# Performance work log

Measured on AMD Instinct MI355X. Metric: run time of the kernel, lower is better.

## Reference

```python
import jax, jax.numpy as jnp
import numpy as np

B, T, D = 2, 2048, 1024
H, DH = 16, 64  # d_model = n_heads * d_head


def setup_inputs() -> dict:
    key = jax.random.key(0)
    k1, k2, k3 = jax.random.split(key, 3)
    x = jax.random.normal(k1, (B, T, D), dtype=jnp.float32)
    # torch Linear(d_model, 3*H*DH, bias=False): store transposed so y = x @ W
    Wqkv = jax.random.normal(k2, (D, 3 * H * DH), dtype=jnp.float32) * (D ** -0.5)
    Wo = jax.random.normal(k3, (H * DH, D), dtype=jnp.float32) * ((H * DH) ** -0.5)
    mask = jnp.ones((B, T), dtype=jnp.float32)  # key padding mask
    return {"x": x, "Wqkv": Wqkv, "Wo": Wo, "mask": mask}


def reference(x, Wqkv, Wo, mask):
    b, t, _ = x.shape
    scale = DH ** -0.5
    qkv = (x @ Wqkv).reshape(b, t, 3, H, DH)
    q = jnp.moveaxis(qkv[:, :, 0], 1, 2)  # [B,H,T,DH]
    k = jnp.moveaxis(qkv[:, :, 1], 1, 2)
    v = jnp.moveaxis(qkv[:, :, 2], 1, 2)
    scores = jnp.einsum('bhqd,bhkd->bhqk', q, k) * scale  # [B,H,T,T]
    causal = jnp.tril(jnp.ones((t, t), dtype=x.dtype))
    # faithful to source: multiply by mask, then fill masked positions with -inf
    scores = scores * causal
    scores = jnp.where(causal == 0, -jnp.inf, scores)
    am = mask[:, None, None, :]  # [B,1,1,T]
    scores = scores * am
    scores = jnp.where(am == 0, -jnp.inf, scores)
    p = jax.nn.softmax(scores, axis=-1)
    p = jnp.where(jnp.isnan(p), jnp.zeros_like(p), p)  # NaN cleanup
    out = jnp.einsum('bhqk,bhkd->bhqd', p, v)
    out = jnp.moveaxis(out, 1, 2).reshape(b, t, H * DH)
    return out @ Wo
```

## Files before the change

### kernel.cpp

```cpp
#include <hip/hip_runtime.h>
#include <math.h>

#define B_ 2
#define T_ 2048
#define D_ 1024
#define H_ 16
#define DH_ 64
#define NROWS (B_ * T_)
#define QKV_N (3 * H_ * DH_)

typedef __attribute__((ext_vector_type(8))) short short8v;
typedef __attribute__((ext_vector_type(4))) float f32x4;

#define SWZ(row) ((((row) & 7) ^ (((row) >> 3) & 7)))
#define GSWZ(row) (((row) >> 1) & 3)

static __device__ __forceinline__ unsigned short f2bf(float x) {
    unsigned u = __float_as_uint(x);
    u = (u + 0x7FFFu + ((u >> 16) & 1u)) >> 16;
    return (unsigned short)u;
}
static __device__ __forceinline__ int packbf(float lo, float hi) {
    return (int)((unsigned)f2bf(lo) | ((unsigned)f2bf(hi) << 16));
}

__global__ __launch_bounds__(256)
void f32_to_bf16_k(const float* __restrict__ in, unsigned short* __restrict__ out,
                   int n8)
{
    const int i = blockIdx.x * 256 + threadIdx.x;
    if (i >= n8) return;
    const float4* p = (const float4*)in;
    float4 a = p[2 * i], b = p[2 * i + 1];
    int4 w;
    w.x = packbf(a.x, a.y); w.y = packbf(a.z, a.w);
    w.z = packbf(b.x, b.y); w.w = packbf(b.z, b.w);
    ((int4*)out)[i] = w;
}

__global__ __launch_bounds__(256)
void transpose_bf16_k(const float* __restrict__ in, unsigned short* __restrict__ out,
                      int R, int C)
{
    __shared__ float tile[64][65];
    const int r0 = blockIdx.y * 64, c0 = blockIdx.x * 64;
    const int tr = threadIdx.x >> 4;
    const int tc = (threadIdx.x & 15) * 4;
#pragma unroll
    for (int rr = 0; rr < 64; rr += 16) {
        float4 v = *(const float4*)(in + (size_t)(r0 + tr + rr) * C + c0 + tc);
        tile[tr + rr][tc + 0] = v.x; tile[tr + rr][tc + 1] = v.y;
        tile[tr + rr][tc + 2] = v.z; tile[tr + rr][tc + 3] = v.w;
    }
    __syncthreads();
    const int ow = threadIdx.x >> 2;
    const int os = (threadIdx.x & 3) * 16;
    int4 w0, w1;
    float s[16];
#pragma unroll
    for (int e = 0; e < 16; ++e) s[e] = tile[os + e][ow];
    w0.x = packbf(s[0], s[1]);   w0.y = packbf(s[2], s[3]);
    w0.z = packbf(s[4], s[5]);   w0.w = packbf(s[6], s[7]);
    w1.x = packbf(s[8], s[9]);   w1.y = packbf(s[10], s[11]);
    w1.z = packbf(s[12], s[13]); w1.w = packbf(s[14], s[15]);
    unsigned short* orow = out + (size_t)(c0 + ow) * R + r0 + os;
    *(int4*)(orow) = w0;
    *(int4*)(orow + 8) = w1;
}

__global__ __launch_bounds__(256)
void gemm_bt_bf16(const unsigned short* __restrict__ A,
                  const unsigned short* __restrict__ Bt,
                  float* __restrict__ C, int M, int N, int K)
{
    __shared__ __align__(16) unsigned short As[2][128 * 32];
    __shared__ __align__(16) unsigned short Bs[2][128 * 32];

    const int tid = threadIdx.x;
    const int w = tid >> 6, l = tid & 63;
    const int lhi = l >> 4, llo = l & 15;
    const int wr = w >> 1, wc = w & 1;
    const int bm = blockIdx.y * 128, bn = blockIdx.x * 128;

    const int srow = w * 32 + (l >> 2);
    const int sg   = l & 3;

    const unsigned short* Ab = A + (size_t)bm * K;
    const unsigned short* Bb = Bt + (size_t)bn * K;

    f32x4 acc[4][4];
#pragma unroll
    for (int mi = 0; mi < 4; ++mi)
#pragma unroll
        for (int ni = 0; ni < 4; ++ni) acc[mi][ni] = (f32x4){0.f, 0.f, 0.f, 0.f};

    short8v a0r, a1r, b0r, b1r;
    const int nt = K >> 5;

#define LOADT(t) do {                                                        \
        const size_t ko = (size_t)(t) * 32 + sg * 8;                         \
        a0r = *(const short8v*)(Ab + (size_t)srow * K + ko);                 \
        a1r = *(const short8v*)(Ab + (size_t)(srow + 16) * K + ko);         \
        b0r = *(const short8v*)(Bb + (size_t)srow * K + ko);                 \
        b1r = *(const short8v*)(Bb + (size_t)(srow + 16) * K + ko);         \
    } while (0)
#define WRITET(buf) do {                                                     \
        *(short8v*)&As[buf][srow * 32 + (sg ^ GSWZ(srow)) * 8] = a0r;        \
        *(short8v*)&As[buf][(srow + 16) * 32 + (sg ^ GSWZ(srow + 16)) * 8] = a1r; \
        *(short8v*)&Bs[buf][srow * 32 + (sg ^ GSWZ(srow)) * 8] = b0r;        \
        *(short8v*)&Bs[buf][(srow + 16) * 32 + (sg ^ GSWZ(srow + 16)) * 8] = b1r; \
    } while (0)

    LOADT(0);
    WRITET(0);
    __syncthreads();

    int cur = 0;
    for (int t = 0; t < nt; ++t) {
        if (t + 1 < nt) LOADT(t + 1);

        short8v af[4], bf[4];
#pragma unroll
        for (int mi = 0; mi < 4; ++mi) {
            const int m = wr * 64 + mi * 16 + llo;
            af[mi] = *(const short8v*)&As[cur][m * 32 + (lhi ^ GSWZ(m)) * 8];
        }
#pragma unroll
        for (int ni = 0; ni < 4; ++ni) {
            const int n = wc * 64 + ni * 16 + llo;
            bf[ni] = *(const short8v*)&Bs[cur][n * 32 + (lhi ^ GSWZ(n)) * 8];
        }
#pragma unroll
        for (int mi = 0; mi < 4; ++mi)
#pragma unroll
            for (int ni = 0; ni < 4; ++ni)
                acc[mi][ni] = __builtin_amdgcn_mfma_f32_16x16x32_bf16(
                    af[mi], bf[ni], acc[mi][ni], 0, 0, 0);

        if (t + 1 < nt) WRITET(cur ^ 1);
        __syncthreads();
        cur ^= 1;
    }
#undef LOADT
#undef WRITET

#pragma unroll
    for (int mi = 0; mi < 4; ++mi)
#pragma unroll
        for (int ni = 0; ni < 4; ++ni) {
            const int col = bn + wc * 64 + ni * 16 + llo;
            const int rb = bm + wr * 64 + mi * 16 + lhi * 4;
#pragma unroll
            for (int i = 0; i < 4; ++i)
                C[(size_t)(rb + i) * N + col] = acc[mi][ni][i];
        }
}

__global__ __launch_bounds__(256)
void attn_mfma(const float* __restrict__ qkv, const float* __restrict__ mask,
               unsigned short* __restrict__ out)
{
    __shared__ __align__(16) unsigned short Ks[64 * 64];
    __shared__ __align__(16) unsigned short Vt[64 * 64];
    __shared__ __align__(16) unsigned short Pl[4][16 * 64];
    __shared__ float ms[64];

    const int tid = threadIdx.x;
    const int w   = tid >> 6;
    const int l   = tid & 63;
    const int lhi = l >> 4;
    const int llo = l & 15;
    const int b = blockIdx.z;
    const int h = blockIdx.y;

    const int sr  = tid >> 2;
    const int sg0 = (tid & 3) * 2;

    for (int qsel = 0; qsel < 2; ++qsel) {
        const int qt = qsel ? (31 - (int)blockIdx.x) : (int)blockIdx.x;
        const int qb = qt * 64;

        short8v qf[2];
        {
            const float* qrow = qkv + (size_t)(b * T_ + qb + w * 16 + llo) * QKV_N
                                + h * DH_;
#pragma unroll
            for (int kc = 0; kc < 2; ++kc) {
                const float* src = qrow + kc * 32 + lhi * 8;
                float4 c0 = *(const float4*)(src);
                float4 c1 = *(const float4*)(src + 4);
                float v[8] = {c0.x, c0.y, c0.z, c0.w, c1.x, c1.y, c1.z, c1.w};
#pragma unroll
                for (int e = 0; e < 8; ++e)
                    qf[kc][e] = (short)f2bf(v[e] * 0.125f);
            }
        }

        f32x4 acc[4];
#pragma unroll
        for (int ct = 0; ct < 4; ++ct) acc[ct] = (f32x4){0.f, 0.f, 0.f, 0.f};
        float mrow[4] = {-INFINITY, -INFINITY, -INFINITY, -INFINITY};
        float lrow[4] = {0.f, 0.f, 0.f, 0.f};

        for (int t0 = 0; t0 <= qt; ++t0) {
            const int k0 = t0 * 64;
            {
                const float* kbase = qkv + (size_t)(b * T_ + k0 + sr) * QKV_N
                                     + H_ * DH_ + h * DH_;
#pragma unroll
                for (int s = 0; s < 2; ++s) {
                    const int g = sg0 + s;
                    float4 ka = *(const float4*)(kbase + g * 8);
                    float4 kb = *(const float4*)(kbase + g * 8 + 4);
                    int4 wk;
                    wk.x = packbf(ka.x, ka.y); wk.y = packbf(ka.z, ka.w);
                    wk.z = packbf(kb.x, kb.y); wk.w = packbf(kb.z, kb.w);
                    *(int4*)&Ks[(sr * 8 + (g ^ SWZ(sr))) * 8] = wk;

                    float4 va = *(const float4*)(kbase + H_ * DH_ + g * 8);
                    float4 vb = *(const float4*)(kbase + H_ * DH_ + g * 8 + 4);
                    float vv[8] = {va.x, va.y, va.z, va.w, vb.x, vb.y, vb.z, vb.w};
#pragma unroll
                    for (int e = 0; e < 8; ++e) {
                        const int dr = g * 8 + e;
                        Vt[(dr * 8 + ((sr >> 3) ^ SWZ(dr))) * 8 + (sr & 7)] =
                            f2bf(vv[e]);
                    }
                }
                if (tid < 64) ms[tid] = mask[b * T_ + k0 + tid];
            }
            __syncthreads();

            float p[4][4];
#pragma unroll
            for (int ct = 0; ct < 4; ++ct) {
                f32x4 a = (f32x4){0.f, 0.f, 0.f, 0.f};
#pragma unroll
                for (int kc = 0; kc < 2; ++kc) {
                    const int row = ct * 16 + llo;
                    const int G = kc * 4 + lhi;
                    short8v kf = *(const short8v*)&Ks[(row * 8 + (G ^ SWZ(row))) * 8];
                    a = __builtin_amdgcn_mfma_f32_16x16x32_bf16(qf[kc], kf, a, 0, 0, 0);
                }
                const int kg = k0 + ct * 16 + llo;
                const float amv = ms[ct * 16 + llo];
#pragma unroll
                for (int i = 0; i < 4; ++i) {
                    const int qg = qb + w * 16 + lhi * 4 + i;
                    const float s = a[i] * amv;
                    p[ct][i] = (kg <= qg && amv != 0.f) ? s : -INFINITY;
                }
            }

            float corr[4], meff[4];
#pragma unroll
            for (int i = 0; i < 4; ++i) {
                float mx = fmaxf(fmaxf(p[0][i], p[1][i]), fmaxf(p[2][i], p[3][i]));
                mx = fmaxf(mx, __shfl_xor(mx, 1));
                mx = fmaxf(mx, __shfl_xor(mx, 2));
                mx = fmaxf(mx, __shfl_xor(mx, 4));
                mx = fmaxf(mx, __shfl_xor(mx, 8));
                const float mn = fmaxf(mrow[i], mx);
                meff[i] = (mn > -INFINITY) ? mn : 0.f;
                corr[i] = __expf(mrow[i] - meff[i]);
                mrow[i] = mn;
            }
#pragma unroll
            for (int i = 0; i < 4; ++i) {
#pragma unroll
                for (int ct = 0; ct < 4; ++ct)
                    p[ct][i] = __expf(p[ct][i] - meff[i]);
                float sm = (p[0][i] + p[1][i]) + (p[2][i] + p[3][i]);
                sm += __shfl_xor(sm, 1);
                sm += __shfl_xor(sm, 2);
                sm += __shfl_xor(sm, 4);
                sm += __shfl_xor(sm, 8);
                lrow[i] = corr[i] * lrow[i] + sm;
#pragma unroll
                for (int ct2 = 0; ct2 < 4; ++ct2)
                    acc[ct2][i] *= corr[i];
            }

            unsigned short* pw = Pl[w];
#pragma unroll
            for (int ct = 0; ct < 4; ++ct) {
                const int c = ct * 16 + llo;
#pragma unroll
                for (int i = 0; i < 4; ++i) {
                    const int r = lhi * 4 + i;
                    pw[(r * 8 + ((c >> 3) ^ SWZ(r))) * 8 + (c & 7)] = f2bf(p[ct][i]);
                }
            }
            asm volatile("s_waitcnt lgkmcnt(0)" ::: "memory");
            __builtin_amdgcn_sched_barrier(0);
            short8v pf[2];
#pragma unroll
            for (int kc = 0; kc < 2; ++kc) {
                const int G = kc * 4 + lhi;
                pf[kc] = *(const short8v*)&pw[(llo * 8 + (G ^ SWZ(llo))) * 8];
            }

#pragma unroll
            for (int ct2 = 0; ct2 < 4; ++ct2) {
#pragma unroll
                for (int kc = 0; kc < 2; ++kc) {
                    const int row = ct2 * 16 + llo;
                    const int G = kc * 4 + lhi;
                    short8v vf = *(const short8v*)&Vt[(row * 8 + (G ^ SWZ(row))) * 8];
                    acc[ct2] = __builtin_amdgcn_mfma_f32_16x16x32_bf16(
                        pf[kc], vf, acc[ct2], 0, 0, 0);
                }
            }
            __syncthreads();
        }

#pragma unroll
        for (int i = 0; i < 4; ++i) {
            const float invl = (lrow[i] > 0.f) ? 1.f / lrow[i] : 0.f;
            const int qg = qb + w * 16 + lhi * 4 + i;
            unsigned short* orow = out + (size_t)(b * T_ + qg) * (H_ * DH_) + h * DH_;
#pragma unroll
            for (int ct2 = 0; ct2 < 4; ++ct2)
                orow[ct2 * 16 + llo] = f2bf(acc[ct2][i] * invl);
        }
    }
}

extern "C" void kernel_launch(void* const* d_in, const int* in_sizes, int n_in,
                              void* d_out, int out_size, void* d_ws, size_t ws_size,
                              hipStream_t stream)
{
    const float* x    = (const float*)d_in[0];
    const float* Wqkv = (const float*)d_in[1];
    const float* Wo   = (const float*)d_in[2];
    const float* mask = (const float*)d_in[3];
    float* out = (float*)d_out;

    char* p = (char*)d_ws;
    float* qkv = (float*)p;                 p += (size_t)NROWS * QKV_N * 4;
    unsigned short* xb      = (unsigned short*)p; p += (size_t)NROWS * D_ * 2;
    unsigned short* wqkv_t  = (unsigned short*)p; p += (size_t)QKV_N * D_ * 2;
    unsigned short* wo_t    = (unsigned short*)p; p += (size_t)D_ * D_ * 2;
    unsigned short* attnb   = (unsigned short*)p;

    f32_to_bf16_k<<<(NROWS * D_ / 8 + 255) / 256, 256, 0, stream>>>(
        x, xb, NROWS * D_ / 8);
    transpose_bf16_k<<<dim3(QKV_N / 64, D_ / 64), 256, 0, stream>>>(
        Wqkv, wqkv_t, D_, QKV_N);
    transpose_bf16_k<<<dim3(D_ / 64, D_ / 64), 256, 0, stream>>>(
        Wo, wo_t, D_, D_);

    gemm_bt_bf16<<<dim3(QKV_N / 128, NROWS / 128), 256, 0, stream>>>(
        xb, wqkv_t, qkv, NROWS, QKV_N, D_);

    attn_mfma<<<dim3(16, H_, B_), 256, 0, stream>>>(qkv, mask, attnb);

    gemm_bt_bf16<<<dim3(D_ / 128, NROWS / 128), 256, 0, stream>>>(
        attnb, wo_t, out, NROWS, D_, H_ * DH_);
}
```

Measured before the change: 251.4 us.

## Fuse QKV epilogue into bf16 head-major Q/K/Vt layouts and prefetch K/V in attention

The QKV GEMM now writes bf16 Q (pre-scaled), K, and transposed V in per-head contiguous layouts instead of a fp32 interleaved buffer. The attention kernel reads these directly with vector loads, register-prefetches the next K/V tile while computing, and launches one q-tile per block (32 blocks in x) instead of pairing two q-tiles per block. This cuts fp32 traffic and per-tile conversion/transposed scatter stores, at the cost of less coalesced epilogue stores in the GEMM and possible causal load imbalance across blocks.

```diff
diff --git a/kernel.cpp b/kernel.cpp
--- a/kernel.cpp
+++ b/kernel.cpp
@@ -69,9 +69,12 @@
 }
 
 __global__ __launch_bounds__(256)
-void gemm_bt_bf16(const unsigned short* __restrict__ A,
-                  const unsigned short* __restrict__ Bt,
-                  float* __restrict__ C, int M, int N, int K)
+void gemm_qkv(const unsigned short* __restrict__ A,
+              const unsigned short* __restrict__ Bt,
+              unsigned short* __restrict__ Qb,
+              unsigned short* __restrict__ Kb,
+              unsigned short* __restrict__ Vtb,
+              int M, int N, int K)
 {
     __shared__ __align__(16) unsigned short As[2][128 * 32];
     __shared__ __align__(16) unsigned short Bs[2][128 * 32];
@@ -118,8 +121,7 @@
     int cur = 0;
     for (int t = 0; t < nt; ++t) {
         if (t + 1 < nt) LOADT(t + 1);
-
-        short8v af[4], bf[4];
+        short8v af[4], bfr[4];
 #pragma unroll
         for (int mi = 0; mi < 4; ++mi) {
             const int m = wr * 64 + mi * 16 + llo;
@@ -128,15 +130,14 @@
 #pragma unroll
         for (int ni = 0; ni < 4; ++ni) {
             const int n = wc * 64 + ni * 16 + llo;
-            bf[ni] = *(const short8v*)&Bs[cur][n * 32 + (lhi ^ GSWZ(n)) * 8];
+            bfr[ni] = *(const short8v*)&Bs[cur][n * 32 + (lhi ^ GSWZ(n)) * 8];
         }
 #pragma unroll
         for (int mi = 0; mi < 4; ++mi)
 #pragma unroll
             for (int ni = 0; ni < 4; ++ni)
                 acc[mi][ni] = __builtin_amdgcn_mfma_f32_16x16x32_bf16(
-                    af[mi], bf[ni], acc[mi][ni], 0, 0, 0);
-
+                    af[mi], bfr[ni], acc[mi][ni], 0, 0, 0);
         if (t + 1 < nt) WRITET(cur ^ 1);
         __syncthreads();
         cur ^= 1;
@@ -149,6 +150,107 @@
 #pragma unroll
         for (int ni = 0; ni < 4; ++ni) {
             const int col = bn + wc * 64 + ni * 16 + llo;
+            const int rb  = bm + wr * 64 + mi * 16 + lhi * 4;
+            const int hh = (col >> 6) & 15;
+            const int dh = col & 63;
+            const int bb = rb >> 11;
+            const int tt = rb & 2047;
+            const int which = col >> 10;
+            if (which == 2) {
+                int2 pk;
+                pk.x = packbf(acc[mi][ni][0], acc[mi][ni][1]);
+                pk.y = packbf(acc[mi][ni][2], acc[mi][ni][3]);
+                *(int2*)&Vtb[((size_t)(bb * H_ + hh) * DH_ + dh) * T_ + tt] = pk;
+            } else {
+                unsigned short* dst = (which == 0 ? Qb : Kb)
+                    + ((size_t)(bb * H_ + hh) * T_ + tt) * DH_ + dh;
+                const float sc = (which == 0) ? 0.125f : 1.f;
+#pragma unroll
+                for (int i = 0; i < 4; ++i)
+                    dst[(size_t)i * DH_] = f2bf(acc[mi][ni][i] * sc);
+            }
+        }
+}
+
+__global__ __launch_bounds__(256)
+void gemm_bt_bf16(const unsigned short* __restrict__ A,
+                  const unsigned short* __restrict__ Bt,
+                  float* __restrict__ C, int M, int N, int K)
+{
+    __shared__ __align__(16) unsigned short As[2][128 * 32];
+    __shared__ __align__(16) unsigned short Bs[2][128 * 32];
+
+    const int tid = threadIdx.x;
+    const int w = tid >> 6, l = tid & 63;
+    const int lhi = l >> 4, llo = l & 15;
+    const int wr = w >> 1, wc = w & 1;
+    const int bm = blockIdx.y * 128, bn = blockIdx.x * 128;
+
+    const int srow = w * 32 + (l >> 2);
+    const int sg   = l & 3;
+
+    const unsigned short* Ab = A + (size_t)bm * K;
+    const unsigned short* Bb = Bt + (size_t)bn * K;
+
+    f32x4 acc[4][4];
+#pragma unroll
+    for (int mi = 0; mi < 4; ++mi)
+#pragma unroll
+        for (int ni = 0; ni < 4; ++ni) acc[mi][ni] = (f32x4){0.f, 0.f, 0.f, 0.f};
+
+    short8v a0r, a1r, b0r, b1r;
+    const int nt = K >> 5;
+
+#define LOADT(t) do {                                                        \
+        const size_t ko = (size_t)(t) * 32 + sg * 8;                         \
+        a0r = *(const short8v*)(Ab + (size_t)srow * K + ko);                 \
+        a1r = *(const short8v*)(Ab + (size_t)(srow + 16) * K + ko);         \
+        b0r = *(const short8v*)(Bb + (size_t)srow * K + ko);                 \
+        b1r = *(const short8v*)(Bb + (size_t)(srow + 16) * K + ko);         \
+    } while (0)
+#define WRITET(buf) do {                                                     \
+        *(short8v*)&As[buf][srow * 32 + (sg ^ GSWZ(srow)) * 8] = a0r;        \
+        *(short8v*)&As[buf][(srow + 16) * 32 + (sg ^ GSWZ(srow + 16)) * 8] = a1r; \
+        *(short8v*)&Bs[buf][srow * 32 + (sg ^ GSWZ(srow)) * 8] = b0r;        \
+        *(short8v*)&Bs[buf][(srow + 16) * 32 + (sg ^ GSWZ(srow + 16)) * 8] = b1r; \
+    } while (0)
+
+    LOADT(0);
+    WRITET(0);
+    __syncthreads();
+
+    int cur = 0;
+    for (int t = 0; t < nt; ++t) {
+        if (t + 1 < nt) LOADT(t + 1);
+        short8v af[4], bfr[4];
+#pragma unroll
+        for (int mi = 0; mi < 4; ++mi) {
+            const int m = wr * 64 + mi * 16 + llo;
+            af[mi] = *(const short8v*)&As[cur][m * 32 + (lhi ^ GSWZ(m)) * 8];
+        }
+#pragma unroll
+        for (int ni = 0; ni < 4; ++ni) {
+            const int n = wc * 64 + ni * 16 + llo;
+            bfr[ni] = *(const short8v*)&Bs[cur][n * 32 + (lhi ^ GSWZ(n)) * 8];
+        }
+#pragma unroll
+        for (int mi = 0; mi < 4; ++mi)
+#pragma unroll
+            for (int ni = 0; ni < 4; ++ni)
+                acc[mi][ni] = __builtin_amdgcn_mfma_f32_16x16x32_bf16(
+                    af[mi], bfr[ni], acc[mi][ni], 0, 0, 0);
+        if (t + 1 < nt) WRITET(cur ^ 1);
+        __syncthreads();
+        cur ^= 1;
+    }
+#undef LOADT
+#undef WRITET
+
+#pragma unroll
+    for (int mi = 0; mi < 4; ++mi)
+#pragma unroll
+        for (int ni = 0; ni < 4; ++ni) {
+            const int col = bn + wc * 64 + ni * 16 + llo;
             const int rb = bm + wr * 64 + mi * 16 + lhi * 4;
 #pragma unroll
             for (int i = 0; i < 4; ++i)
@@ -156,173 +258,166 @@
         }
 }
 
-__global__ __launch_bounds__(256)
-void attn_mfma(const float* __restrict__ qkv, const float* __restrict__ mask,
+__global__ __launch_bounds__(256, 4)
+void attn_mfma(const unsigned short* __restrict__ Qb,
+               const unsigned short* __restrict__ Kb,
+               const unsigned short* __restrict__ Vtb,
+               const float* __restrict__ mask,
                unsigned short* __restrict__ out)
 {
     __shared__ __align__(16) unsigned short Ks[64 * 64];
-    __shared__ __align__(16) unsigned short Vt[64 * 64];
+    __shared__ __align__(16) unsigned short Vs[64 * 64];
     __shared__ __align__(16) unsigned short Pl[4][16 * 64];
     __shared__ float ms[64];
 
     const int tid = threadIdx.x;
-    const int w   = tid >> 6;
-    const int l   = tid & 63;
-    const int lhi = l >> 4;
-    const int llo = l & 15;
-    const int b = blockIdx.z;
-    const int h = blockIdx.y;
+    const int w = tid >> 6, l = tid & 63;
+    const int lhi = l >> 4, llo = l & 15;
+    const int qt = 31 - (int)blockIdx.x;
+    const int b = blockIdx.z, h = blockIdx.y;
+    const int qb = qt * 64;
+
+    const size_t bh = (size_t)(b * H_ + h);
+    const unsigned short* Kbase = Kb + bh * T_ * DH_;
+    const unsigned short* Vbase = Vtb + bh * DH_ * T_;
 
     const int sr  = tid >> 2;
     const int sg0 = (tid & 3) * 2;
 
-    for (int qsel = 0; qsel < 2; ++qsel) {
-        const int qt = qsel ? (31 - (int)blockIdx.x) : (int)blockIdx.x;
-        const int qb = qt * 64;
-
-        short8v qf[2];
+    short8v qf[2];
+    {
+        const unsigned short* qrow = Qb + (bh * T_ + qb + w * 16 + llo) * DH_;
+        qf[0] = *(const short8v*)(qrow + lhi * 8);
+        qf[1] = *(const short8v*)(qrow + 32 + lhi * 8);
+    }
+
+    f32x4 acc[4];
+#pragma unroll
+    for (int ct = 0; ct < 4; ++ct) acc[ct] = (f32x4){0.f, 0.f, 0.f, 0.f};
+    float mrow[4] = {-INFINITY, -INFINITY, -INFINITY, -INFINITY};
+    float lrow[4] = {0.f, 0.f, 0.f, 0.f};
+
+    int4 kr0, kr1, vr0, vr1;
+    float mval;
+#define LOADKV(t) do {                                                       \
+        const int kk = (t) * 64;                                             \
+        const unsigned short* kp = Kbase + (size_t)(kk + sr) * DH_ + sg0 * 8;\
+        kr0 = *(const int4*)(kp);                                            \
+        kr1 = *(const int4*)(kp + 8);                                        \
+        const unsigned short* vp = Vbase + (size_t)sr * T_ + kk + sg0 * 8;   \
+        vr0 = *(const int4*)(vp);                                            \
+        vr1 = *(const int4*)(vp + 8);                                        \
+        mval = (tid < 64) ? mask[b * T_ + kk + tid] : 0.f;                   \
+    } while (0)
+
+    LOADKV(0);
+
+    for (int t0 = 0; t0 <= qt; ++t0) {
+        const int k0 = t0 * 64;
+        *(int4*)&Ks[(sr * 8 + (sg0 ^ SWZ(sr))) * 8] = kr0;
+        *(int4*)&Ks[(sr * 8 + ((sg0 + 1) ^ SWZ(sr))) * 8] = kr1;
+        *(int4*)&Vs[(sr * 8 + (sg0 ^ SWZ(sr))) * 8] = vr0;
+        *(int4*)&Vs[(sr * 8 + ((sg0 + 1) ^ SWZ(sr))) * 8] = vr1;
+        if (tid < 64) ms[tid] = mval;
+        __syncthreads();
+
         {
-            const float* qrow = qkv + (size_t)(b * T_ + qb + w * 16 + llo) * QKV_N
-                                + h * DH_;
+            const int tn = (t0 < qt) ? t0 + 1 : 0;
+            LOADKV(tn);
+        }
+
+        float p[4][4];
+#pragma unroll
+        for (int ct = 0; ct < 4; ++ct) {
+            f32x4 a = (f32x4){0.f, 0.f, 0.f, 0.f};
 #pragma unroll
             for (int kc = 0; kc < 2; ++kc) {
-                const float* src = qrow + kc * 32 + lhi * 8;
-                float4 c0 = *(const float4*)(src);
-                float4 c1 = *(const float4*)(src + 4);
-                float v[8] = {c0.x, c0.y, c0.z, c0.w, c1.x, c1.y, c1.z, c1.w};
-#pragma unroll
-                for (int e = 0; e < 8; ++e)
-                    qf[kc][e] = (short)f2bf(v[e] * 0.125f);
+                const int row = ct * 16 + llo;
+                const int G = kc * 4 + lhi;
+                short8v kf = *(const short8v*)&Ks[(row * 8 + (G ^ SWZ(row))) * 8];
+                a = __builtin_amdgcn_mfma_f32_16x16x32_bf16(qf[kc], kf, a, 0, 0, 0);
             }
-        }
-
-        f32x4 acc[4];
-#pragma unroll
-        for (int ct = 0; ct < 4; ++ct) acc[ct] = (f32x4){0.f, 0.f, 0.f, 0.f};
-        float mrow[4] = {-INFINITY, -INFINITY, -INFINITY, -INFINITY};
-        float lrow[4] = {0.f, 0.f, 0.f, 0.f};
-
-        for (int t0 = 0; t0 <= qt; ++t0) {
-            const int k0 = t0 * 64;
-            {
-                const float* kbase = qkv + (size_t)(b * T_ + k0 + sr) * QKV_N
-                                     + H_ * DH_ + h * DH_;
-#pragma unroll
-                for (int s = 0; s < 2; ++s) {
-                    const int g = sg0 + s;
-                    float4 ka = *(const float4*)(kbase + g * 8);
-                    float4 kb = *(const float4*)(kbase + g * 8 + 4);
-                    int4 wk;
-                    wk.x = packbf(ka.x, ka.y); wk.y = packbf(ka.z, ka.w);
-                    wk.z = packbf(kb.x, kb.y); wk.w = packbf(kb.z, kb.w);
-                    *(int4*)&Ks[(sr * 8 + (g ^ SWZ(sr))) * 8] = wk;
-
-                    float4 va = *(const float4*)(kbase + H_ * DH_ + g * 8);
-                    float4 vb = *(const float4*)(kbase + H_ * DH_ + g * 8 + 4);
-                    float vv[8] = {va.x, va.y, va.z, va.w, vb.x, vb.y, vb.z, vb.w};
-#pragma unroll
-                    for (int e = 0; e < 8; ++e) {
-                        const int dr = g * 8 + e;
-                        Vt[(dr * 8 + ((sr >> 3) ^ SWZ(dr))) * 8 + (sr & 7)] =
-                            f2bf(vv[e]);
-                    }
-                }
-                if (tid < 64) ms[tid] = mask[b * T_ + k0 + tid];
+            const int kg = k0 + ct * 16 + llo;
+            const float amv = ms[ct * 16 + llo];
+#pragma unroll
+            for (int i = 0; i < 4; ++i) {
+                const int qg = qb + w * 16 + lhi * 4 + i;
+                const float s = a[i] * amv;
+                p[ct][i] = (kg <= qg && amv != 0.f) ? s : -INFINITY;
             }
-            __syncthreads();
-
-            float p[4][4];
-#pragma unroll
-            for (int ct = 0; ct < 4; ++ct) {
-                f32x4 a = (f32x4){0.f, 0.f, 0.f, 0.f};
-#pragma unroll
-                for (int kc = 0; kc < 2; ++kc) {
-                    const int row = ct * 16 + llo;
-                    const int G = kc * 4 + lhi;
-                    short8v kf = *(const short8v*)&Ks[(row * 8 + (G ^ SWZ(row))) * 8];
-                    a = __builtin_amdgcn_mfma_f32_16x16x32_bf16(qf[kc], kf, a, 0, 0, 0);
-                }
-                const int kg = k0 + ct * 16 + llo;
-                const float amv = ms[ct * 16 + llo];
-#pragma unroll
-                for (int i = 0; i < 4; ++i) {
-                    const int qg = qb + w * 16 + lhi * 4 + i;
-                    const float s = a[i] * amv;
-                    p[ct][i] = (kg <= qg && amv != 0.f) ? s : -INFINITY;
-                }
+        }
+
+        float corr[4], meff[4];
+#pragma unroll
+        for (int i = 0; i < 4; ++i) {
+            float mx = fmaxf(fmaxf(p[0][i], p[1][i]), fmaxf(p[2][i], p[3][i]));
+            mx = fmaxf(mx, __shfl_xor(mx, 1));
+            mx = fmaxf(mx, __shfl_xor(mx, 2));
+            mx = fmaxf(mx, __shfl_xor(mx, 4));
+            mx = fmaxf(mx, __shfl_xor(mx, 8));
+            const float mn = fmaxf(mrow[i], mx);
+            meff[i] = (mn > -INFINITY) ? mn : 0.f;
+            corr[i] = __expf(mrow[i] - meff[i]);
+            mrow[i] = mn;
+        }
+#pragma unroll
+        for (int i = 0; i < 4; ++i) {
+#pragma unroll
+            for (int ct = 0; ct < 4; ++ct)
+                p[ct][i] = __expf(p[ct][i] - meff[i]);
+            float sm = (p[0][i] + p[1][i]) + (p[2][i] + p[3][i]);
+            sm += __shfl_xor(sm, 1);
+            sm += __shfl_xor(sm, 2);
+            sm += __shfl_xor(sm, 4);
+            sm += __shfl_xor(sm, 8);
+            lrow[i] = corr[i] * lrow[i] + sm;
+#pragma unroll
+            for (int ct2 = 0; ct2 < 4; ++ct2)
+                acc[ct2][i] *= corr[i];
+        }
+
+        unsigned short* pw = Pl[w];
+#pragma unroll
+        for (int ct = 0; ct < 4; ++ct) {
+            const int c = ct * 16 + llo;
+#pragma unroll
+            for (int i = 0; i < 4; ++i) {
+                const int r = lhi * 4 + i;
+                pw[(r * 8 + ((c >> 3) ^ SWZ(r))) * 8 + (c & 7)] = f2bf(p[ct][i]);
             }
-
-            float corr[4], meff[4];
-#pragma unroll
-            for (int i = 0; i < 4; ++i) {
-                float mx = fmaxf(fmaxf(p[0][i], p[1][i]), fmaxf(p[2][i], p[3][i]));
-                mx = fmaxf(mx, __shfl_xor(mx, 1));
-                mx = fmaxf(mx, __shfl_xor(mx, 2));
-                mx = fmaxf(mx, __shfl_xor(mx, 4));
-                mx = fmaxf(mx, __shfl_xor(mx, 8));
-                const float mn = fmaxf(mrow[i], mx);
-                meff[i] = (mn > -INFINITY) ? mn : 0.f;
-                corr[i] = __expf(mrow[i] - meff[i]);
-                mrow[i] = mn;
+        }
+        asm volatile("s_waitcnt lgkmcnt(0)" ::: "memory");
+        __builtin_amdgcn_sched_barrier(0);
+        short8v pf[2];
+#pragma unroll
+        for (int kc = 0; kc < 2; ++kc) {
+            const int G = kc * 4 + lhi;
+            pf[kc] = *(const short8v*)&pw[(llo * 8 + (G ^ SWZ(llo))) * 8];
+        }
+
+#pragma unroll
+        for (int ct2 = 0; ct2 < 4; ++ct2) {
+#pragma unroll
+            for (int kc = 0; kc < 2; ++kc) {
+                const int row = ct2 * 16 + llo;
+                const int G = kc * 4 + lhi;
+                short8v vf = *(const short8v*)&Vs[(row * 8 + (G ^ SWZ(row))) * 8];
+                acc[ct2] = __builtin_amdgcn_mfma_f32_16x16x32_bf16(
+                    pf[kc], vf, acc[ct2], 0, 0, 0);
             }
-#pragma unroll
-            for (int i = 0; i < 4; ++i) {
-#pragma unroll
-                for (int ct = 0; ct < 4; ++ct)
-                    p[ct][i] = __expf(p[ct][i] - meff[i]);
-                float sm = (p[0][i] + p[1][i]) + (p[2][i] + p[3][i]);
-                sm += __shfl_xor(sm, 1);
-                sm += __shfl_xor(sm, 2);
-                sm += __shfl_xor(sm, 4);
-                sm += __shfl_xor(sm, 8);
-                lrow[i] = corr[i] * lrow[i] + sm;
-#pragma unroll
-                for (int ct2 = 0; ct2 < 4; ++ct2)
-                    acc[ct2][i] *= corr[i];
-            }
-
-            unsigned short* pw = Pl[w];
-#pragma unroll
-            for (int ct = 0; ct < 4; ++ct) {
-                const int c = ct * 16 + llo;
-#pragma unroll
-                for (int i = 0; i < 4; ++i) {
-                    const int r = lhi * 4 + i;
-                    pw[(r * 8 + ((c >> 3) ^ SWZ(r))) * 8 + (c & 7)] = f2bf(p[ct][i]);
-                }
-            }
-            asm volatile("s_waitcnt lgkmcnt(0)" ::: "memory");
-            __builtin_amdgcn_sched_barrier(0);
-            short8v pf[2];
-#pragma unroll
-            for (int kc = 0; kc < 2; ++kc) {
-                const int G = kc * 4 + lhi;
-                pf[kc] = *(const short8v*)&pw[(llo * 8 + (G ^ SWZ(llo))) * 8];
-            }
-
-#pragma unroll
-            for (int ct2 = 0; ct2 < 4; ++ct2) {
-#pragma unroll
-                for (int kc = 0; kc < 2; ++kc) {
-                    const int row = ct2 * 16 + llo;
-                    const int G = kc * 4 + lhi;
-                    short8v vf = *(const short8v*)&Vt[(row * 8 + (G ^ SWZ(row))) * 8];
-                    acc[ct2] = __builtin_amdgcn_mfma_f32_16x16x32_bf16(
-                        pf[kc], vf, acc[ct2], 0, 0, 0);
-                }
-            }
-            __syncthreads();
-        }
-
-#pragma unroll
-        for (int i = 0; i < 4; ++i) {
-            const float invl = (lrow[i] > 0.f) ? 1.f / lrow[i] : 0.f;
-            const int qg = qb + w * 16 + lhi * 4 + i;
-            unsigned short* orow = out + (size_t)(b * T_ + qg) * (H_ * DH_) + h * DH_;
-#pragma unroll
-            for (int ct2 = 0; ct2 < 4; ++ct2)
-                orow[ct2 * 16 + llo] = f2bf(acc[ct2][i] * invl);
-        }
+        }
+        __syncthreads();
+    }
+#undef LOADKV
+
+#pragma unroll
+    for (int i = 0; i < 4; ++i) {
+        const float invl = (lrow[i] > 0.f) ? 1.f / lrow[i] : 0.f;
+        const int qg = qb + w * 16 + lhi * 4 + i;
+        unsigned short* orow = out + (size_t)(b * T_ + qg) * (H_ * DH_) + h * DH_;
+#pragma unroll
+        for (int ct2 = 0; ct2 < 4; ++ct2)
+            orow[ct2 * 16 + llo] = f2bf(acc[ct2][i] * invl);
     }
 }
 
@@ -337,11 +432,13 @@
     float* out = (float*)d_out;
 
     char* p = (char*)d_ws;
-    float* qkv = (float*)p;                 p += (size_t)NROWS * QKV_N * 4;
-    unsigned short* xb      = (unsigned short*)p; p += (size_t)NROWS * D_ * 2;
-    unsigned short* wqkv_t  = (unsigned short*)p; p += (size_t)QKV_N * D_ * 2;
-    unsigned short* wo_t    = (unsigned short*)p; p += (size_t)D_ * D_ * 2;
-    unsigned short* attnb   = (unsigned short*)p;
+    unsigned short* xb     = (unsigned short*)p; p += (size_t)NROWS * D_ * 2;
+    unsigned short* wqkv_t = (unsigned short*)p; p += (size_t)QKV_N * D_ * 2;
+    unsigned short* wo_t   = (unsigned short*)p; p += (size_t)D_ * D_ * 2;
+    unsigned short* Qb     = (unsigned short*)p; p += (size_t)NROWS * D_ * 2;
+    unsigned short* Kb     = (unsigned short*)p; p += (size_t)NROWS * D_ * 2;
+    unsigned short* Vtb    = (unsigned short*)p; p += (size_t)NROWS * D_ * 2;
+    unsigned short* attnb  = (unsigned short*)p;
 
     f32_to_bf16_k<<<(NROWS * D_ / 8 + 255) / 256, 256, 0, stream>>>(
         x, xb, NROWS * D_ / 8);
@@ -350,10 +447,10 @@
     transpose_bf16_k<<<dim3(D_ / 64, D_ / 64), 256, 0, stream>>>(
         Wo, wo_t, D_, D_);
 
-    gemm_bt_bf16<<<dim3(QKV_N / 128, NROWS / 128), 256, 0, stream>>>(
-        xb, wqkv_t, qkv, NROWS, QKV_N, D_);
-
-    attn_mfma<<<dim3(16, H_, B_), 256, 0, stream>>>(qkv, mask, attnb);
+    gemm_qkv<<<dim3(QKV_N / 128, NROWS / 128), 256, 0, stream>>>(
+        xb, wqkv_t, Qb, Kb, Vtb, NROWS, QKV_N, D_);
+
+    attn_mfma<<<dim3(32, H_, B_), 256, 0, stream>>>(Qb, Kb, Vtb, mask, attnb);
 
     gemm_bt_bf16<<<dim3(D_ / 128, NROWS / 128), 256, 0, stream>>>(
         attnb, wo_t, out, NROWS, D_, H_ * DH_);
```

Result: slower. 256.9 us (+2.2%).
